# Kernel optimization log

Hardware: AMD Instinct MI355X
Metric: run time of the kernel (lower is better)

The kernel has to match this reference:

```python
import jax, jax.numpy as jnp
import numpy as np
from jax import lax

K = 9
ISHAPE = (2048, 2048)
STRIDES = (4, 8, 16, 32)
NUM_ROIS = 300
IOU_THR = 0.5
SCORE_THR = 0.5
PRE_NMS_TOPK = 4000  # standard pre-NMS candidate cap; keeps suppression loop small


def _make_anchors(h, w, stride):
    scales = np.array([1.0, 2.0, 4.0]) * 4.0 * stride
    ratios = np.sqrt(np.array([0.5, 1.0, 2.0]))
    ah = (scales[:, None] * ratios[None, :]).reshape(-1)   # (9,)
    aw = (scales[:, None] / ratios[None, :]).reshape(-1)
    cy = (np.arange(h, dtype=np.float32) + 0.5) * stride
    cx = (np.arange(w, dtype=np.float32) + 0.5) * stride
    cy, cx = np.meshgrid(cy, cx, indexing='ij')             # (h,w)
    y1 = cy[..., None] - 0.5 * ah
    x1 = cx[..., None] - 0.5 * aw
    y2 = cy[..., None] + 0.5 * ah
    x2 = cx[..., None] + 0.5 * aw
    return np.stack([y1, x1, y2, x2], axis=-1).astype(np.float32)  # (h,w,9,4)


def setup_inputs() -> dict:
    key = jax.random.key(0)
    ks = jax.random.split(key, 4)
    sizes = [(512, 512), (256, 256), (128, 128), (64, 64)]
    out = {}
    for i, ((h, w), s, k) in enumerate(zip(sizes, STRIDES, ks), start=1):
        out[f'x{i}'] = jax.random.uniform(k, (1, h, w, 6 * K), dtype=jnp.float32)
        out[f'anchors{i}'] = jnp.asarray(_make_anchors(h, w, s))
    return out


def _decode_level(clzbbe, anchors):
    # clzbbe: (h,w,6k) -> (h,w,k,6); channels per anchor: [fg, bg, dy, dx, dh, dw]
    h, w, k, _ = anchors.shape
    t = clzbbe.reshape(h, w, k, 6)
    scores = t[..., 0]
    dy, dx, dh, dw = t[..., 2], t[..., 3], t[..., 4], t[..., 5]
    ah = anchors[..., 2] - anchors[..., 0]
    aw = anchors[..., 3] - anchors[..., 1]
    acy = anchors[..., 0] + 0.5 * ah
    acx = anchors[..., 1] + 0.5 * aw
    cy = acy + dy * ah
    cx = acx + dx * aw
    bh = ah * jnp.exp(dh)
    bw = aw * jnp.exp(dw)
    y1 = jnp.clip(cy - 0.5 * bh, 0.0, float(ISHAPE[0]))
    x1 = jnp.clip(cx - 0.5 * bw, 0.0, float(ISHAPE[1]))
    y2 = jnp.clip(cy + 0.5 * bh, 0.0, float(ISHAPE[0]))
    x2 = jnp.clip(cx + 0.5 * bw, 0.0, float(ISHAPE[1]))
    boxes = jnp.stack([y1, x1, y2, x2], axis=-1).reshape(-1, 4)
    return boxes, scores.reshape(-1)


def _iou_one_vs_all(box, boxes):
    yy1 = jnp.maximum(box[0], boxes[:, 0])
    xx1 = jnp.maximum(box[1], boxes[:, 1])
    yy2 = jnp.minimum(box[2], boxes[:, 2])
    xx2 = jnp.minimum(box[3], boxes[:, 3])
    inter = jnp.maximum(yy2 - yy1, 0.0) * jnp.maximum(xx2 - xx1, 0.0)
    a1 = (box[2] - box[0]) * (box[3] - box[1])
    a2 = (boxes[:, 2] - boxes[:, 0]) * (boxes[:, 3] - boxes[:, 1])
    return inter / (a1 + a2 - inter + 1e-9)


def _pnsm(boxes, scores):
    # pre-NMS top-k candidates
    top_scores, top_idx = lax.top_k(scores, PRE_NMS_TOPK)
    cand_boxes = boxes[top_idx]                              # (TOPK, 4)
    s0 = jnp.where(top_scores >= SCORE_THR, top_scores, -1.0)

    def step(s, _):
        i = jnp.argmax(s)
        best_score = s[i]
        best_box = cand_boxes[i]
        iou = _iou_one_vs_all(best_box, cand_boxes)
        s = jnp.where(iou > IOU_THR, -1.0, s).at[i].set(-1.0)
        roi = jnp.where(best_score > 0.0, best_box, jnp.zeros_like(best_box))
        return s, roi

    _, rois = lax.scan(step, s0, None, length=NUM_ROIS)      # (NUM_ROIS, 4)
    return rois


def reference(x1, x2, x3, x4, anchors1, anchors2, anchors3, anchors4):
    levels = [(x1[0], anchors1), (x2[0], anchors2), (x3[0], anchors3), (x4[0], anchors4)]
    decoded = [_decode_level(c, a) for c, a in levels]
    boxes = jnp.concatenate([b for b, _ in decoded], axis=0)   # (N, 4)
    scores = jnp.concatenate([s for _, s in decoded], axis=0)  # (N,)
    rois = _pnsm(boxes, scores)
    return rois[None]                                          # (1, NUM_ROIS, 4)
```

## Files before the change

kernel.cpp:

```cpp
#include <hip/hip_runtime.h>


namespace {

constexpr int kNTot = 3133440;
constexpr int kB1 = 2359296;
constexpr int kB2 = 2949120;
constexpr int kB3 = 3096576;
constexpr int kNBins = 8192;
constexpr int kNParts = 256;
constexpr int kCap = 8192;
constexpr int kTopK = 4000;
constexpr int kNPad = 4096;
constexpr int kNRois = 300;
constexpr int kJChunk = 2048;
constexpr int kITile = 256;
constexpr int kBCS = 16;

constexpr int kF4L[4] = {3538944, 884736, 221184, 55296};
constexpr int kLvlB0[5] = {0, 193, 241, 253, 256};
constexpr int kLvlAB[4] = {0, kB1, kB2, kB3};

struct LevelPick { const float* x; unsigned local; };

__device__ __forceinline__ LevelPick pick_level(unsigned g, const float* x1, const float* x2,
                                                const float* x3, const float* x4) {
  LevelPick p;
  if (g < (unsigned)kB1)      { p.x = x1; p.local = g; }
  else if (g < (unsigned)kB2) { p.x = x2; p.local = g - kB1; }
  else if (g < (unsigned)kB3) { p.x = x3; p.local = g - kB2; }
  else                        { p.x = x4; p.local = g - kB3; }
  return p;
}

__device__ __forceinline__ int score_bin(float s) {
  int b = (int)(s * (float)kNBins);
  return min(max(b, 0), kNBins - 1);
}

__device__ __forceinline__ void load_scores4(const float* x, unsigned local0, float s[4]) {
  const float4* p = (const float4*)(x + (size_t)local0 * 6);
  float4 q0 = p[0], q1 = p[1], q3 = p[3], q4 = p[4];
  s[0] = q0.x; s[1] = q1.z; s[2] = q3.x; s[3] = q4.z;
}

__global__ __launch_bounds__(1024) void hist_kernel(
    const float4* __restrict__ x1, const float4* __restrict__ x2,
    const float4* __restrict__ x3, const float4* __restrict__ x4,
    unsigned* __restrict__ part, float* __restrict__ scores) {
  __shared__ unsigned h[kNBins];
  for (int i = threadIdx.x; i < kNBins; i += 1024) h[i] = 0;
  __syncthreads();
  const int bid = blockIdx.x;
  int lvl = (bid < kLvlB0[1]) ? 0 : (bid < kLvlB0[2]) ? 1 : (bid < kLvlB0[3]) ? 2 : 3;
  const float4* x = (lvl == 0) ? x1 : (lvl == 1) ? x2 : (lvl == 2) ? x3 : x4;
  const int nf4 = kF4L[lvl];
  const int abase = kLvlAB[lvl];
  const int bloc = bid - kLvlB0[lvl];
  const int nblk = kLvlB0[lvl + 1] - kLvlB0[lvl];
  for (int q = bloc * 1024 + threadIdx.x; q < nf4; q += nblk * 1024) {
    float4 v = x[q];
    int qd = q / 3;
    int r = q - qd * 3;
    if (r != 2) {
      float s = (r == 0) ? v.x : v.z;
      atomicAdd(&h[score_bin(s)], 1u);
      if (scores) scores[abase + 2 * qd + r] = s;
    }
  }
  __syncthreads();
  for (int i = threadIdx.x; i < kNBins; i += 1024)
    part[blockIdx.x * kNBins + i] = h[i];
}

__global__ void reduce_kernel(const unsigned* __restrict__ part, unsigned* __restrict__ hist) {
  int b = blockIdx.x * 256 + threadIdx.x;
  unsigned t0 = 0, t1 = 0, t2 = 0, t3 = 0;
  for (int p = 0; p < kNParts; p += 4) {
    t0 += part[(size_t)(p + 0) * kNBins + b];
    t1 += part[(size_t)(p + 1) * kNBins + b];
    t2 += part[(size_t)(p + 2) * kNBins + b];
    t3 += part[(size_t)(p + 3) * kNBins + b];
  }
  hist[b] = t0 + t1 + t2 + t3;
}

__global__ __launch_bounds__(1024) void select_kernel(
    const unsigned* __restrict__ hist, unsigned* __restrict__ sel,
    unsigned* __restrict__ counter, unsigned* __restrict__ binStart) {
  __shared__ unsigned wtot[16];
  __shared__ unsigned maxB;
  const int t = threadIdx.x;
  const int lane = t & 63;
  const int wv = t >> 6;
  if (t == 0) maxB = 0u;
  unsigned h[8];
  unsigned s = 0;
  #pragma unroll
  for (int i = 0; i < 8; ++i) { h[i] = hist[t * 8 + i]; s += h[i]; }
  unsigned p = s;
  #pragma unroll
  for (int off = 1; off < 64; off <<= 1) {
    unsigned n = __shfl_up(p, off);
    if (lane >= off) p += n;
  }
  if (lane == 63) wtot[wv] = p;
  __syncthreads();
  if (wv == 0 && lane < 16) {
    unsigned wp = wtot[lane];
    #pragma unroll
    for (int off = 1; off < 16; off <<= 1) {
      unsigned n = __shfl_up(wp, off);
      if (lane >= off) wp += n;
    }
    wtot[lane] = wp;
  }
  __syncthreads();
  const unsigned total = wtot[15];
  const unsigned Pincl = p + (wv > 0 ? wtot[wv - 1] : 0u);
  const unsigned T = total - Pincl;
  unsigned bs[8];
  bs[7] = T;
  #pragma unroll
  for (int i = 6; i >= 0; --i) bs[i] = bs[i + 1] + h[i + 1];
  #pragma unroll
  for (int i = 0; i < 8; ++i) binStart[t * 8 + i] = bs[i];
  unsigned cand = 0;
  #pragma unroll
  for (int i = 0; i < 8; ++i)
    if (bs[i] + h[i] >= (unsigned)kTopK) cand = (unsigned)(t * 8 + i);
  atomicMax(&maxB, cand);
  __syncthreads();
  const unsigned B = maxB;
  if (t == (int)(B >> 3)) {
    unsigned i = B & 7u;
    unsigned n = bs[i] + h[i];
    sel[0] = B;
    counter[0] = n < (unsigned)kCap ? n : (unsigned)kCap;
  }
}

__device__ __forceinline__ void try_append(float s, unsigned g, unsigned B,
                                           const unsigned* __restrict__ binStart,
                                           unsigned* __restrict__ binCount,
                                           unsigned long long* __restrict__ keys) {
  unsigned bin = (unsigned)score_bin(s);
  if (bin >= B) {
    unsigned pos = binStart[bin] + atomicAdd(&binCount[bin << 4], 1u);
    if (pos < (unsigned)kCap) {
      keys[pos] = ((unsigned long long)__float_as_uint(s) << 32) |
                  (unsigned long long)(0xFFFFFFFFu - g);
    }
  }
}

__global__ void compact_s_kernel(const float4* __restrict__ scores4,
                                 const unsigned* __restrict__ sel,
                                 const unsigned* __restrict__ binStart,
                                 unsigned* __restrict__ binCount,
                                 unsigned long long* __restrict__ keys) {
  int t = blockIdx.x * blockDim.x + threadIdx.x;
  if (t >= kNTot / 4) return;
  float4 v = scores4[t];
  unsigned g0 = (unsigned)t * 4;
  unsigned B = sel[0];
  try_append(v.x, g0 + 0, B, binStart, binCount, keys);
  try_append(v.y, g0 + 1, B, binStart, binCount, keys);
  try_append(v.z, g0 + 2, B, binStart, binCount, keys);
  try_append(v.w, g0 + 3, B, binStart, binCount, keys);
}

__global__ void compact_x_kernel(const float* __restrict__ x1, const float* __restrict__ x2,
                                 const float* __restrict__ x3, const float* __restrict__ x4,
                                 const unsigned* __restrict__ sel,
                                 const unsigned* __restrict__ binStart,
                                 unsigned* __restrict__ binCount,
                                 unsigned long long* __restrict__ keys) {
  int t = blockIdx.x * blockDim.x + threadIdx.x;
  if (t >= kNTot / 4) return;
  unsigned g0 = (unsigned)t * 4;
  LevelPick lp = pick_level(g0, x1, x2, x3, x4);
  float s[4];
  load_scores4(lp.x, lp.local, s);
  unsigned B = sel[0];
  #pragma unroll
  for (int i = 0; i < 4; ++i) try_append(s[i], g0 + i, B, binStart, binCount, keys);
}

__global__ void rank_kernel(const unsigned long long* __restrict__ keys,
                            const unsigned* __restrict__ counter,
                            unsigned* __restrict__ rankArr) {
  __shared__ unsigned long long lk[kJChunk];
  int n = (int)*counter;
  int itile = blockIdx.x / (kCap / kJChunk);
  int jc = blockIdx.x % (kCap / kJChunk);
  int i0 = itile * kITile;
  int j0 = jc * kJChunk;
  if (i0 >= n || j0 >= n) return;
  for (int j = threadIdx.x; j < kJChunk; j += kITile) {
    int jj = j0 + j;
    lk[j] = (jj < n) ? keys[jj] : 0ull;
  }
  __syncthreads();
  int i = i0 + threadIdx.x;
  unsigned long long ki = (i < n) ? keys[i] : ~0ull;
  int r0 = 0, r1 = 0, r2 = 0, r3 = 0;
  const ulonglong2* p2 = (const ulonglong2*)lk;
  #pragma unroll 4
  for (int j = 0; j < kJChunk / 8; ++j) {
    ulonglong2 a = p2[j];
    ulonglong2 b = p2[256 + j];
    ulonglong2 c = p2[512 + j];
    ulonglong2 d = p2[768 + j];
    r0 += (int)(a.x > ki) + (int)(a.y > ki);
    r1 += (int)(b.x > ki) + (int)(b.y > ki);
    r2 += (int)(c.x > ki) + (int)(c.y > ki);
    r3 += (int)(d.x > ki) + (int)(d.y > ki);
  }
  if (i < n) atomicAdd(&rankArr[i], (unsigned)(r0 + r1 + r2 + r3));
}

__global__ void scatter_kernel(const unsigned long long* __restrict__ keys,
                               const unsigned* __restrict__ counter,
                               const unsigned* __restrict__ rankArr,
                               unsigned long long* __restrict__ sorted) {
  int i = blockIdx.x * 256 + threadIdx.x;
  int n = (int)*counter;
  if (i < n) {
    unsigned r = rankArr[i];
    if (r < (unsigned)kNPad) sorted[r] = keys[i];
  }
}

__device__ __forceinline__ void decode_box(unsigned g,
                                           const float* __restrict__ x1, const float* __restrict__ x2,
                                           const float* __restrict__ x3, const float* __restrict__ x4,
                                           const float* __restrict__ a1, const float* __restrict__ a2,
                                           const float* __restrict__ a3, const float* __restrict__ a4,
                                           float4* box) {
  const float* x;
  const float* anc;
  unsigned local;
  if (g < (unsigned)kB1)      { x = x1; anc = a1; local = g; }
  else if (g < (unsigned)kB2) { x = x2; anc = a2; local = g - kB1; }
  else if (g < (unsigned)kB3) { x = x3; anc = a3; local = g - kB2; }
  else                        { x = x4; anc = a4; local = g - kB3; }
  const float* xe = x + (size_t)local * 6;
  float dy = xe[2], dx = xe[3], dh = xe[4], dwv = xe[5];
  const float* ae = anc + (size_t)local * 4;
  float ay1 = ae[0], ax1 = ae[1], ay2 = ae[2], ax2 = ae[3];
  float ah = ay2 - ay1;
  float aw = ax2 - ax1;
  float acy = ay1 + 0.5f * ah;
  float acx = ax1 + 0.5f * aw;
  float cy = acy + dy * ah;
  float cx = acx + dx * aw;
  float bh = ah * expf(dh);
  float bw = aw * expf(dwv);
  box->x = fminf(fmaxf(cy - 0.5f * bh, 0.0f), 2048.0f);
  box->y = fminf(fmaxf(cx - 0.5f * bw, 0.0f), 2048.0f);
  box->z = fminf(fmaxf(cy + 0.5f * bh, 0.0f), 2048.0f);
  box->w = fminf(fmaxf(cx + 0.5f * bw, 0.0f), 2048.0f);
}

__global__ void decode_kernel(const unsigned long long* __restrict__ sorted,
                              const unsigned* __restrict__ counter,
                              const float* __restrict__ x1, const float* __restrict__ x2,
                              const float* __restrict__ x3, const float* __restrict__ x4,
                              const float* __restrict__ a1, const float* __restrict__ a2,
                              const float* __restrict__ a3, const float* __restrict__ a4,
                              float4* __restrict__ boxes,
                              unsigned long long* __restrict__ supinit) {
  int r = blockIdx.x * 256 + threadIdx.x;
  int n = min((int)*counter, kTopK);
  unsigned long long key = (r < n) ? sorted[r] : 0ull;
  float4 box = make_float4(0.f, 0.f, 0.f, 0.f);
  float sc = 0.f;
  if (key != 0ull) {
    sc = __uint_as_float((unsigned)(key >> 32));
    unsigned g = 0xFFFFFFFFu - (unsigned)(key & 0xFFFFFFFFull);
    if (g < (unsigned)kNTot) decode_box(g, x1, x2, x3, x4, a1, a2, a3, a4, &box);
  }
  boxes[r] = box;
  unsigned long long dead = __ballot(!(sc >= 0.5f));
  if ((threadIdx.x & 63) == 0) supinit[r >> 6] = dead;
}

__global__ void iou_kernel(const float4* __restrict__ boxes,
                           unsigned long long* __restrict__ rows,
                           unsigned long long* __restrict__ diag) {
  int wave = (blockIdx.x * blockDim.x + threadIdx.x) >> 6;
  int lane = threadIdx.x & 63;
  if (wave >= kTopK * 64) return;
  int row = wave >> 6;
  int wc = wave & 63;
  if (wc < (row >> 6)) return;
  int j = wc * 64 + lane;
  float4 bi = boxes[row];
  float4 bj = boxes[j];
  float yy1 = fmaxf(bi.x, bj.x);
  float xx1 = fmaxf(bi.y, bj.y);
  float yy2 = fminf(bi.z, bj.z);
  float xx2 = fminf(bi.w, bj.w);
  float inter = fmaxf(yy2 - yy1, 0.0f) * fmaxf(xx2 - xx1, 0.0f);
  float ar1 = (bi.z - bi.x) * (bi.w - bi.y);
  float ar2 = (bj.z - bj.x) * (bj.w - bj.y);
  float iou = inter / (ar1 + ar2 - inter + 1e-9f);
  unsigned long long m = __ballot(iou > 0.5f);
  if (lane == 0) {
    rows[(size_t)row * 64 + wc] = m;
    if (wc == (row >> 6)) diag[row] = m;
  }
}

__device__ __forceinline__ void glds16(const void* g, void* l) {
  __builtin_amdgcn_global_load_lds(
      (const __attribute__((address_space(1))) unsigned int*)g,
      (__attribute__((address_space(3))) unsigned int*)l, 16, 0, 0);
}

__global__ __launch_bounds__(64, 1) void greedy_kernel(
    const float4* __restrict__ boxes,
    const unsigned long long* __restrict__ supinit,
    const unsigned long long* __restrict__ rows,
    const unsigned long long* __restrict__ diag,
    float* __restrict__ out) {
  __shared__ unsigned long long diagL[kNPad];
  __shared__ unsigned long long slots[16][128];
  __shared__ int picksLds[kNRois];
  const int lane = threadIdx.x;

  {
    const char* src = (const char*)diag;
    char* dst = (char*)diagL;
    #pragma unroll
    for (int i = 0; i < 32; ++i)
      glds16(src + i * 1024 + lane * 16, dst + i * 1024);
  }
  unsigned long long remv = supinit[lane];
  asm volatile("s_waitcnt vmcnt(0)" ::: "memory");
  __builtin_amdgcn_sched_barrier(0);

  int count = 0;
  for (int W = 0; W < 64; ++W) {
    unsigned long long alive = ~__shfl(remv, W);
    if (alive == 0ull) continue;
    unsigned long long dw = diagL[(W << 6) + lane];
    const int bank = (W & 1) << 3;
    int pend = 0;
    while (alive != 0ull && count < kNRois) {
      const int i = __builtin_ctzll(alive);
      const int r = (W << 6) + i;
      if (lane == 0) picksLds[count] = r;
      ++count;
      if (pend == 8) {
        asm volatile("s_waitcnt vmcnt(0)" ::: "memory");
        __builtin_amdgcn_sched_barrier(0);
        #pragma unroll
        for (int k = 0; k < 8; ++k) remv |= slots[bank + k][lane];
        asm volatile("s_waitcnt lgkmcnt(0)" ::: "memory");
        __builtin_amdgcn_sched_barrier(0);
        pend = 0;
      }
      glds16((const char*)(rows + ((size_t)r << 6)) + lane * 16,
             (char*)&slots[bank + pend][0]);
      ++pend;
      unsigned long long d = __shfl(dw, i);
      alive &= ~(d | (1ull << i));
    }
    asm volatile("s_waitcnt vmcnt(0)" ::: "memory");
    __builtin_amdgcn_sched_barrier(0);
    for (int k = 0; k < pend; ++k) remv |= slots[bank + k][lane];
    if (count >= kNRois) break;
    unsigned long long ahead = (lane > W) ? ~remv : 0ull;
    if (__ballot(ahead != 0ull) == 0ull) break;
  }

  for (int p = lane; p < kNRois; p += 64) {
    float4 bx = make_float4(0.f, 0.f, 0.f, 0.f);
    if (p < count) bx = boxes[picksLds[p]];
    ((float4*)out)[p] = bx;
  }
}

}

extern "C" void kernel_launch(void* const* d_in, const int* in_sizes, int n_in,
                              void* d_out, int out_size, void* d_ws, size_t ws_size,
                              hipStream_t stream) {
  const float* x1 = (const float*)d_in[0];
  const float* a1 = (const float*)d_in[1];
  const float* x2 = (const float*)d_in[2];
  const float* a2 = (const float*)d_in[3];
  const float* x3 = (const float*)d_in[4];
  const float* a3 = (const float*)d_in[5];
  const float* x4 = (const float*)d_in[6];
  const float* a4 = (const float*)d_in[7];

  char* ws = (char*)d_ws;
  size_t off = 0;
  unsigned* part = (unsigned*)(ws + off);       off += (size_t)kNParts * kNBins * 4;
  unsigned* hist = (unsigned*)(ws + off);       off += kNBins * 4;
  unsigned* counter = (unsigned*)(ws + off);    off += 4;
  unsigned* sel = (unsigned*)(ws + off);        off += 4;
  unsigned* rankArr = (unsigned*)(ws + off);    off += (size_t)kCap * 4;
  unsigned* binCount = (unsigned*)(ws + off);   off += (size_t)kNBins * kBCS * 4;
  unsigned* binStart = (unsigned*)(ws + off);   off += (size_t)kNBins * 4;
  unsigned long long* supinit = (unsigned long long*)(ws + off);  off += 512 + 8;
  unsigned long long* sorted = (unsigned long long*)(ws + off);   off += (size_t)kNPad * 8;
  unsigned long long* keys = (unsigned long long*)(ws + off);     off += (size_t)kCap * 8;
  float4* boxes = (float4*)(ws + off);          off += (size_t)kNPad * 16;
  unsigned long long* rows = (unsigned long long*)(ws + off);     off += (size_t)kTopK * 64 * 8;
  unsigned long long* diag = (unsigned long long*)(ws + off);     off += (size_t)kNPad * 8;
  const bool sidecar = ws_size >= off + (size_t)kNTot * 4;
  float* scores = sidecar ? (float*)(ws + off) : nullptr;
  float* out = (float*)d_out;

  hipMemsetAsync((void*)counter, 0, 8 + (size_t)kCap * 4 + (size_t)kNBins * kBCS * 4,
                 stream);

  hist_kernel<<<kNParts, 1024, 0, stream>>>(
      (const float4*)x1, (const float4*)x2, (const float4*)x3, (const float4*)x4,
      part, scores);
  reduce_kernel<<<kNBins / 256, 256, 0, stream>>>(part, hist);
  select_kernel<<<1, 1024, 0, stream>>>(hist, sel, counter, binStart);
  int blocks4 = (kNTot / 4 + 255) / 256;
  if (sidecar) {
    compact_s_kernel<<<blocks4, 256, 0, stream>>>(
        (const float4*)scores, sel, binStart, binCount, keys);
  } else {
    compact_x_kernel<<<blocks4, 256, 0, stream>>>(
        x1, x2, x3, x4, sel, binStart, binCount, keys);
  }
  rank_kernel<<<(kCap / kITile) * (kCap / kJChunk), kITile, 0, stream>>>(
      keys, counter, rankArr);
  scatter_kernel<<<kCap / 256, 256, 0, stream>>>(keys, counter, rankArr, sorted);
  decode_kernel<<<kNPad / 256, 256, 0, stream>>>(
      sorted, counter, x1, x2, x3, x4, a1, a2, a3, a4, boxes, supinit);
  iou_kernel<<<(kTopK * 64 * 64) / 256, 256, 0, stream>>>(boxes, rows, diag);
  greedy_kernel<<<1, 64, 0, stream>>>(boxes, supinit, rows, diag, out);
}
```

Measured before the change: 144.9 us.

## Process greedy NMS in 256-candidate blocks with register-resident diagonal band

The IoU kernel now writes a 4-word diagonal band per row (the 256x256 block around the diagonal) instead of a single diagonal word. The greedy kernel keeps the current and next band blocks in registers and resolves suppression within four consecutive words per block. This means the global-row merges and wait barriers happen once per 256 candidates instead of once per 64. It also raises the pending-slot count to 16 and prefetches the next band, replacing the up-front LDS copy of the whole diagonal. The cost is more register pressure, more shuffles per pick, and a larger diagonal buffer written by the IoU kernel.

```diff
diff --git a/kernel.cpp b/kernel.cpp
--- a/kernel.cpp
+++ b/kernel.cpp
@@ -16,6 +16,7 @@
 constexpr int kJChunk = 2048;
 constexpr int kITile = 256;
 constexpr int kBCS = 16;
+constexpr int kSlots = 16;
 
 constexpr int kF4L[4] = {3538944, 884736, 221184, 55296};
 constexpr int kLvlB0[5] = {0, 193, 241, 253, 256};
@@ -288,7 +289,7 @@
 
 __global__ void iou_kernel(const float4* __restrict__ boxes,
                            unsigned long long* __restrict__ rows,
-                           unsigned long long* __restrict__ diag) {
+                           unsigned long long* __restrict__ diagband) {
   int wave = (blockIdx.x * blockDim.x + threadIdx.x) >> 6;
   int lane = threadIdx.x & 63;
   if (wave >= kTopK * 64) return;
@@ -309,7 +310,7 @@
   unsigned long long m = __ballot(iou > 0.5f);
   if (lane == 0) {
     rows[(size_t)row * 64 + wc] = m;
-    if (wc == (row >> 6)) diag[row] = m;
+    if ((wc >> 2) == (row >> 8)) diagband[(size_t)row * 4 + (wc & 3)] = m;
   }
 }
 
@@ -323,58 +324,88 @@
     const float4* __restrict__ boxes,
     const unsigned long long* __restrict__ supinit,
     const unsigned long long* __restrict__ rows,
-    const unsigned long long* __restrict__ diag,
+    const unsigned long long* __restrict__ diagband,
     float* __restrict__ out) {
-  __shared__ unsigned long long diagL[kNPad];
-  __shared__ unsigned long long slots[16][128];
+  __shared__ unsigned long long slots[kSlots][128];
   __shared__ int picksLds[kNRois];
   const int lane = threadIdx.x;
-
-  {
-    const char* src = (const char*)diag;
-    char* dst = (char*)diagL;
+  unsigned long long remv = supinit[lane];
+
+  const ulonglong2* dbp = (const ulonglong2*)diagband;
+  unsigned long long bandC[4][4], bandN[4][4];
+  #pragma unroll
+  for (int s = 0; s < 4; ++s) {
+    ulonglong2 t0 = dbp[(size_t)((s << 6) + lane) * 2 + 0];
+    ulonglong2 t1 = dbp[(size_t)((s << 6) + lane) * 2 + 1];
+    bandC[s][0] = t0.x; bandC[s][1] = t0.y; bandC[s][2] = t1.x; bandC[s][3] = t1.y;
+  }
+
+  int count = 0;
+
+#define PROCESS_WORD(J, AJ, ...)                                         \
+    while (AJ != 0ull && count < kNRois) {                               \
+      const int i = __builtin_ctzll(AJ);                                 \
+      const int r = (B << 8) + (J << 6) + i;                             \
+      if (lane == 0) picksLds[count] = r;                                \
+      ++count;                                                           \
+      if (pend == kSlots) {                                              \
+        asm volatile("s_waitcnt vmcnt(0)" ::: "memory");                 \
+        __builtin_amdgcn_sched_barrier(0);                               \
+        _Pragma("unroll")                                                \
+        for (int k = 0; k < kSlots; ++k) remv |= slots[k][lane];         \
+        asm volatile("s_waitcnt lgkmcnt(0)" ::: "memory");               \
+        __builtin_amdgcn_sched_barrier(0);                               \
+        pend = 0;                                                        \
+      }                                                                  \
+      glds16((const char*)(rows + ((size_t)r << 6)) + lane * 16,         \
+             (char*)&slots[pend][0]);                                    \
+      ++pend;                                                            \
+      unsigned long long s0 = __shfl(bandC[J][0], i);                    \
+      unsigned long long s1 = __shfl(bandC[J][1], i);                    \
+      unsigned long long s2 = __shfl(bandC[J][2], i);                    \
+      unsigned long long s3 = __shfl(bandC[J][3], i);                    \
+      (void)s0; (void)s1; (void)s2; (void)s3;                            \
+      __VA_ARGS__                                                        \
+      AJ &= ~(1ull << i);                                                \
+      if (lane == ((B << 2) + J)) remv |= 1ull << i;                     \
+    }
+
+  for (int B = 0; B < 16; ++B) {
+    const int Bn = (B + 1 < 16) ? B + 1 : 15;
     #pragma unroll
-    for (int i = 0; i < 32; ++i)
-      glds16(src + i * 1024 + lane * 16, dst + i * 1024);
-  }
-  unsigned long long remv = supinit[lane];
-  asm volatile("s_waitcnt vmcnt(0)" ::: "memory");
-  __builtin_amdgcn_sched_barrier(0);
-
-  int count = 0;
-  for (int W = 0; W < 64; ++W) {
-    unsigned long long alive = ~__shfl(remv, W);
-    if (alive == 0ull) continue;
-    unsigned long long dw = diagL[(W << 6) + lane];
-    const int bank = (W & 1) << 3;
+    for (int s = 0; s < 4; ++s) {
+      ulonglong2 t0 = dbp[(size_t)((Bn << 8) + (s << 6) + lane) * 2 + 0];
+      ulonglong2 t1 = dbp[(size_t)((Bn << 8) + (s << 6) + lane) * 2 + 1];
+      bandN[s][0] = t0.x; bandN[s][1] = t0.y; bandN[s][2] = t1.x; bandN[s][3] = t1.y;
+    }
+
+    unsigned long long a0 = ~__shfl(remv, (B << 2) + 0);
+    unsigned long long a1 = ~__shfl(remv, (B << 2) + 1);
+    unsigned long long a2 = ~__shfl(remv, (B << 2) + 2);
+    unsigned long long a3 = ~__shfl(remv, (B << 2) + 3);
     int pend = 0;
-    while (alive != 0ull && count < kNRois) {
-      const int i = __builtin_ctzll(alive);
-      const int r = (W << 6) + i;
-      if (lane == 0) picksLds[count] = r;
-      ++count;
-      if (pend == 8) {
-        asm volatile("s_waitcnt vmcnt(0)" ::: "memory");
-        __builtin_amdgcn_sched_barrier(0);
-        #pragma unroll
-        for (int k = 0; k < 8; ++k) remv |= slots[bank + k][lane];
-        asm volatile("s_waitcnt lgkmcnt(0)" ::: "memory");
-        __builtin_amdgcn_sched_barrier(0);
-        pend = 0;
-      }
-      glds16((const char*)(rows + ((size_t)r << 6)) + lane * 16,
-             (char*)&slots[bank + pend][0]);
-      ++pend;
-      unsigned long long d = __shfl(dw, i);
-      alive &= ~(d | (1ull << i));
-    }
+
+    PROCESS_WORD(0, a0, a0 &= ~s0; a1 &= ~s1; a2 &= ~s2; a3 &= ~s3;)
+    PROCESS_WORD(1, a1, a1 &= ~s1; a2 &= ~s2; a3 &= ~s3;)
+    PROCESS_WORD(2, a2, a2 &= ~s2; a3 &= ~s3;)
+    PROCESS_WORD(3, a3, a3 &= ~s3;)
+
     asm volatile("s_waitcnt vmcnt(0)" ::: "memory");
     __builtin_amdgcn_sched_barrier(0);
-    for (int k = 0; k < pend; ++k) remv |= slots[bank + k][lane];
+    for (int k = 0; k < pend; ++k) remv |= slots[k][lane];
+    asm volatile("s_waitcnt lgkmcnt(0)" ::: "memory");
+    __builtin_amdgcn_sched_barrier(0);
     if (count >= kNRois) break;
-    unsigned long long ahead = (lane > W) ? ~remv : 0ull;
+    unsigned long long ahead = (lane > ((B << 2) + 3)) ? ~remv : 0ull;
     if (__ballot(ahead != 0ull) == 0ull) break;
-  }
+
+    #pragma unroll
+    for (int s = 0; s < 4; ++s) {
+      bandC[s][0] = bandN[s][0]; bandC[s][1] = bandN[s][1];
+      bandC[s][2] = bandN[s][2]; bandC[s][3] = bandN[s][3];
+    }
+  }
+#undef PROCESS_WORD
 
   for (int p = lane; p < kNRois; p += 64) {
     float4 bx = make_float4(0.f, 0.f, 0.f, 0.f);
@@ -411,7 +442,7 @@
   unsigned long long* keys = (unsigned long long*)(ws + off);     off += (size_t)kCap * 8;
   float4* boxes = (float4*)(ws + off);          off += (size_t)kNPad * 16;
   unsigned long long* rows = (unsigned long long*)(ws + off);     off += (size_t)kTopK * 64 * 8;
-  unsigned long long* diag = (unsigned long long*)(ws + off);     off += (size_t)kNPad * 8;
+  unsigned long long* diagband = (unsigned long long*)(ws + off); off += (size_t)kNPad * 4 * 8;
   const bool sidecar = ws_size >= off + (size_t)kNTot * 4;
   float* scores = sidecar ? (float*)(ws + off) : nullptr;
   float* out = (float*)d_out;
@@ -437,6 +468,6 @@
   scatter_kernel<<<kCap / 256, 256, 0, stream>>>(keys, counter, rankArr, sorted);
   decode_kernel<<<kNPad / 256, 256, 0, stream>>>(
       sorted, counter, x1, x2, x3, x4, a1, a2, a3, a4, boxes, supinit);
-  iou_kernel<<<(kTopK * 64 * 64) / 256, 256, 0, stream>>>(boxes, rows, diag);
-  greedy_kernel<<<1, 64, 0, stream>>>(boxes, supinit, rows, diag, out);
-}
+  iou_kernel<<<(kTopK * 64 * 64) / 256, 256, 0, stream>>>(boxes, rows, diagband);
+  greedy_kernel<<<1, 64, 0, stream>>>(boxes, supinit, rows, diagband, out);
+}
```

After: 152.2 us. +5.1%, slower.
